# Kernel tuning notes

Hardware: AMD Instinct MI355X
Metric: run time of the kernel (lower is better)

## Reference

```python
import jax, jax.numpy as jnp
import numpy as np

B, N, D, H = 4, 4096, 1024, 16
HD = D // H  # head dim = 64


def setup_inputs() -> dict:
    key = jax.random.key(0)
    k1, k2, k3 = jax.random.split(key, 3)
    x = jax.random.normal(k1, (B, N, D), dtype=jnp.float32)
    Wqkv = jax.random.normal(k2, (3 * D, D), dtype=jnp.float32) * (1.0 / np.sqrt(D))
    Wo = jax.random.normal(k3, (D, D), dtype=jnp.float32) * (1.0 / np.sqrt(D))
    bo = jnp.zeros((D,), dtype=jnp.float32)
    return {"x": x, "Wqkv": Wqkv, "Wo": Wo, "bo": bo}


def reference(x, Wqkv, Wo, bo):
    # qkv projection (no bias): [B,N,3D] -> [B,N,3,H,HD]
    qkv = jnp.einsum('bnd,ed->bne', x, Wqkv).reshape(B, N, 3, H, HD)
    q, k, v = qkv[:, :, 0], qkv[:, :, 1], qkv[:, :, 2]  # each [B,N,H,HD]
    # NOTE: faithful to source — heads are NOT moved to a batch axis, so
    # scores are [B,N,H,H]: attention mixes across heads per token.
    scores = jnp.einsum('bnhd,bngd->bnhg', q, k) / jnp.sqrt(jnp.float32(D))
    w = jax.nn.softmax(scores, axis=-1)            # [B,N,H,H]
    attn = jnp.einsum('bnhg,bngd->bnhd', w, v)     # [B,N,H,HD]
    attn = attn.reshape(B, N, D)
    return jnp.einsum('bnd,ed->bne', attn, Wo) + bo
```

## Files before the change

kernel.cpp:

```cpp
#include <hip/hip_runtime.h>
#include <hip/hip_bf16.h>

using bf16 = __hip_bfloat16;
typedef __attribute__((ext_vector_type(8))) short bf16x8;
typedef __attribute__((ext_vector_type(4))) float f32x4;

#define GLL(gp, lp) __builtin_amdgcn_global_load_lds( \
    (const __attribute__((address_space(1))) void*)(gp), \
    (__attribute__((address_space(3))) void*)(lp), 16, 0, 0)

#define BAR()    asm volatile("s_barrier" ::: "memory")
#define WAITV4() asm volatile("s_waitcnt vmcnt(4)" ::: "memory")
#define WAITV0() asm volatile("s_waitcnt vmcnt(0)" ::: "memory")
#define WAITL0() do { asm volatile("s_waitcnt lgkmcnt(0)" ::: "memory"); \
                      __builtin_amdgcn_sched_barrier(0); } while (0)

__device__ inline short bfbits(float f) {
  union { bf16 h; short s; } u;
  u.h = __float2bfloat16(f);
  return u.s;
}

__device__ inline bf16x8 ldcvt(const float* __restrict__ g) {
  const float4 f0 = *(const float4*)(g);
  const float4 f1 = *(const float4*)(g + 4);
  union { short s[8]; bf16x8 v; } u;
  u.s[0] = bfbits(f0.x); u.s[1] = bfbits(f0.y); u.s[2] = bfbits(f0.z); u.s[3] = bfbits(f0.w);
  u.s[4] = bfbits(f1.x); u.s[5] = bfbits(f1.y); u.s[6] = bfbits(f1.z); u.s[7] = bfbits(f1.w);
  return u.v;
}

__device__ inline void store_c(float* C, size_t idx, float v) { C[idx] = v; }
__device__ inline void store_c(bf16*  C, size_t idx, float v) { C[idx] = __float2bfloat16(v); }

__global__ __launch_bounds__(256)
void f32_to_bf16(const float* __restrict__ src, bf16* __restrict__ dst, int n8) {
  const int i = blockIdx.x * 256 + threadIdx.x;
  if (i < n8) *(bf16x8*)(dst + (size_t)i * 8) = ldcvt(src + (size_t)i * 8);
}

template <typename TB, typename TC>
__global__ __launch_bounds__(256)
void gemm_nt(const bf16* __restrict__ A, const TB* __restrict__ B,
             const float* __restrict__ bias, TC* __restrict__ C,
             int K, int lda, int ldb, int ldc) {
  constexpr bool B_F32 = sizeof(TB) == 4;
  __shared__ __align__(16) bf16 As[128 * 32];
  __shared__ __align__(16) bf16 Bs[128 * 32];
  const int tid  = threadIdx.x;
  const int lane = tid & 63;
  const int wave = tid >> 6;
  const int wm = wave >> 1, wn = wave & 1;
  const int m0 = blockIdx.y * 128;
  const int n0 = blockIdx.x * 128;

  const int srow = wave * 16 + (lane >> 2);
  const int scol = (lane & 3) * 8;
  const bf16* gA0 = A + (size_t)(m0 + srow) * lda + scol;
  const bf16* gA1 = A + (size_t)(m0 + 64 + srow) * lda + scol;
  const TB*   gB0 = B + (size_t)(n0 + srow) * ldb + scol;
  const TB*   gB1 = B + (size_t)(n0 + 64 + srow) * ldb + scol;
  bf16* lA0 = &As[(wave * 16) * 32];
  bf16* lA1 = lA0 + 64 * 32;
  bf16* lB0u = &Bs[(wave * 16) * 32];
  bf16* lB1u = lB0u + 64 * 32;
  bf16* lB0p = &Bs[srow * 32 + scol];
  bf16* lB1p = lB0p + 64 * 32;

  const int fr = lane & 15;
  const int kq = (lane >> 4) * 8;
  f32x4 acc[4][4] = {};

  for (int k0 = 0; k0 < K; k0 += 32) {
    bf16x8 b0, b1;
    if constexpr (B_F32) {
      b0 = ldcvt((const float*)gB0 + k0);
      b1 = ldcvt((const float*)gB1 + k0);
    }
    __syncthreads();
    GLL(gA0 + k0, lA0);
    GLL(gA1 + k0, lA1);
    if constexpr (B_F32) {
      *(bf16x8*)lB0p = b0;
      *(bf16x8*)lB1p = b1;
    } else {
      GLL((const bf16*)gB0 + k0, lB0u);
      GLL((const bf16*)gB1 + k0, lB1u);
    }
    __syncthreads();
    bf16x8 af[4], bfv[4];
#pragma unroll
    for (int t = 0; t < 4; ++t) {
      af[t]  = *(const bf16x8*)&As[(wm * 64 + t * 16 + fr) * 32 + kq];
      bfv[t] = *(const bf16x8*)&Bs[(wn * 64 + t * 16 + fr) * 32 + kq];
    }
#pragma unroll
    for (int i = 0; i < 4; ++i)
#pragma unroll
      for (int j = 0; j < 4; ++j)
        acc[i][j] = __builtin_amdgcn_mfma_f32_16x16x32_bf16(af[i], bfv[j], acc[i][j], 0, 0, 0);
  }

  const int rq  = (lane >> 4) * 4;
  const int col = lane & 15;
#pragma unroll
  for (int j = 0; j < 4; ++j) {
    const int cn = n0 + wn * 64 + j * 16 + col;
    const float bv = bias ? bias[cn] : 0.0f;
#pragma unroll
    for (int i = 0; i < 4; ++i) {
      const int cm = m0 + wm * 64 + i * 16 + rq;
#pragma unroll
      for (int r = 0; r < 4; ++r)
        store_c(C, (size_t)(cm + r) * ldc + cn, acc[i][j][r] + bv);
    }
  }
}

template <typename TC>
__global__ __launch_bounds__(512)
void gemm256(const bf16* __restrict__ A, const bf16* __restrict__ B,
             const float* __restrict__ bias, TC* __restrict__ C,
             int K, int lda, int ldb, int ldc, int nbx) {
  __shared__ __align__(16) bf16 As[2][256][64];
  __shared__ __align__(16) bf16 Bs[2][256][64];
  const int tid  = threadIdx.x;
  const int lane = tid & 63;
  const int wave = tid >> 6;
  const int wm = wave >> 2;
  const int wn = wave & 3;

  int wg = blockIdx.x;
  const int nwg = gridDim.x;
  if ((nwg & 7) == 0) wg = (wg & 7) * (nwg >> 3) + (wg >> 3);
  const int m0 = (wg / nbx) * 256;
  const int n0 = (wg % nbx) * 256;

  const int srow = wave * 8 + (lane >> 3);
  const int scol = ((lane & 7) ^ (lane >> 3)) * 8;
  const bf16* gA = A + (size_t)(m0 + srow) * lda + scol;
  const bf16* gB = B + (size_t)(n0 + srow) * ldb + scol;

  const int fr = lane & 15, quad = lane >> 4, swz = fr & 7;

#define STAGE_A(buf, h, kt) do { \
    GLL(gA + (size_t)((h) * 128     ) * lda + (kt) * 64, &As[buf][(h) * 128      + wave * 8][0]); \
    GLL(gA + (size_t)((h) * 128 + 64) * lda + (kt) * 64, &As[buf][(h) * 128 + 64 + wave * 8][0]); \
  } while (0)
#define STAGE_B(buf, h, kt) do { \
    GLL(gB + (size_t)((h) * 128     ) * ldb + (kt) * 64, &Bs[buf][(h) * 128      + wave * 8][0]); \
    GLL(gB + (size_t)((h) * 128 + 64) * ldb + (kt) * 64, &Bs[buf][(h) * 128 + 64 + wave * 8][0]); \
  } while (0)
#define LDA_G(buf, mh) do { _Pragma("unroll") \
    for (int t = 0; t < 4; ++t) { _Pragma("unroll") \
      for (int ks = 0; ks < 2; ++ks) \
        av[t * 2 + ks] = *(const bf16x8*)&As[buf][wm * 128 + (mh) * 64 + t * 16 + fr] \
                                            [(((ks << 2) | quad) ^ swz) << 3]; } } while (0)
#define LDB_G(buf, nh, dst) do { _Pragma("unroll") \
    for (int t = 0; t < 2; ++t) { _Pragma("unroll") \
      for (int ks = 0; ks < 2; ++ks) \
        dst[t * 2 + ks] = *(const bf16x8*)&Bs[buf][wn * 64 + (nh) * 32 + t * 16 + fr] \
                                             [(((ks << 2) | quad) ^ swz) << 3]; } } while (0)
#define MFMA_Q(mh, nh, bb) do { \
    __builtin_amdgcn_s_setprio(1); \
    _Pragma("unroll") \
    for (int t = 0; t < 4; ++t) { _Pragma("unroll") \
      for (int u = 0; u < 2; ++u) { _Pragma("unroll") \
        for (int ks = 0; ks < 2; ++ks) \
          acc[(mh) * 4 + t][(nh) * 2 + u] = __builtin_amdgcn_mfma_f32_16x16x32_bf16( \
              av[t * 2 + ks], bb[u * 2 + ks], acc[(mh) * 4 + t][(nh) * 2 + u], 0, 0, 0); } } \
    __builtin_amdgcn_s_setprio(0); } while (0)

  bf16x8 av[8], b0[4], b1[4];
  f32x4 acc[8][4] = {};

  STAGE_A(0, 0, 0); STAGE_A(0, 1, 0);
  STAGE_B(0, 0, 0); STAGE_B(0, 1, 0);
  STAGE_B(1, 0, 1); STAGE_B(1, 1, 1);
  WAITV4(); BAR();

  const int KT = K >> 6;
  const int NI = KT >> 1;
  for (int i = 0; i < NI; ++i) {
    const int kt1 = 2 * i + 1;
    const int ka  = (2 * i + 2 < KT) ? 2 * i + 2 : 0;
    const int kb  = (2 * i + 3 < KT) ? 2 * i + 3 : 0;

    LDA_G(0, 0); LDB_G(0, 0, b0); STAGE_A(1, 0, kt1);
    BAR(); WAITL0(); MFMA_Q(0, 0, b0); BAR();
    LDB_G(0, 1, b1); STAGE_A(1, 1, kt1);
    BAR(); WAITL0(); MFMA_Q(0, 1, b1); BAR();
    LDA_G(0, 1); STAGE_B(0, 0, ka);
    BAR(); WAITL0(); MFMA_Q(1, 1, b1); BAR();
    STAGE_B(0, 1, ka); WAITV4();
    BAR(); WAITL0(); MFMA_Q(1, 0, b0); BAR();
    LDA_G(1, 0); LDB_G(1, 0, b0); STAGE_A(0, 0, ka);
    BAR(); WAITL0(); MFMA_Q(0, 0, b0); BAR();
    LDB_G(1, 1, b1); STAGE_A(0, 1, ka);
    BAR(); WAITL0(); MFMA_Q(0, 1, b1); BAR();
    LDA_G(1, 1); STAGE_B(1, 0, kb);
    BAR(); WAITL0(); MFMA_Q(1, 1, b1); BAR();
    STAGE_B(1, 1, kb); WAITV4();
    BAR(); WAITL0(); MFMA_Q(1, 0, b0); BAR();
  }
  WAITV0();

  const int rq = quad * 4;
#pragma unroll
  for (int nj = 0; nj < 4; ++nj) {
    const int cn = n0 + wn * 64 + nj * 16 + fr;
    const float bv = bias ? bias[cn] : 0.0f;
#pragma unroll
    for (int mi = 0; mi < 8; ++mi) {
      const int cm = m0 + wm * 128 + mi * 16 + rq;
#pragma unroll
      for (int r = 0; r < 4; ++r)
        store_c(C, (size_t)(cm + r) * ldc + cn, acc[mi][nj][r] + bv);
    }
  }
#undef STAGE_A
#undef STAGE_B
#undef LDA_G
#undef LDB_G
#undef MFMA_Q
}

__global__ __launch_bounds__(256)
void attn_heads(bf16* __restrict__ qkv) {
  __shared__ __align__(16) bf16  s_qkv[4][3072];
  __shared__ __align__(16) float s_w[4][256];
  const int lane = threadIdx.x & 63;
  const int wave = threadIdx.x >> 6;
  const size_t tok = (size_t)blockIdx.x * 4 + wave;
  bf16* grow = qkv + tok * 3072;

#pragma unroll
  for (int i = 0; i < 6; ++i) {
    const int off = (i * 64 + lane) * 8;
    *(uint4*)(&s_qkv[wave][off]) = *(const uint4*)(&grow[off]);
  }
  __syncthreads();

  const bf16* sq = s_qkv[wave];
  const int fr   = lane & 15;
  const int quad = lane >> 4;

  f32x4 sc = {0.f, 0.f, 0.f, 0.f};
#pragma unroll
  for (int c = 0; c < 2; ++c) {
    bf16x8 a = *(const bf16x8*)&sq[fr * 64 + c * 32 + quad * 8];
    bf16x8 b = *(const bf16x8*)&sq[1024 + fr * 64 + c * 32 + quad * 8];
    sc = __builtin_amdgcn_mfma_f32_16x16x32_bf16(a, b, sc, 0, 0, 0);
  }

#pragma unroll
  for (int r = 0; r < 4; ++r) {
    float s = sc[r] * 0.03125f;
    float mx = s;
#pragma unroll
    for (int msk = 1; msk < 16; msk <<= 1) mx = fmaxf(mx, __shfl_xor(mx, msk, 64));
    float e = __expf(s - mx);
    float sum = e;
#pragma unroll
    for (int msk = 1; msk < 16; msk <<= 1) sum += __shfl_xor(sum, msk, 64);
    s_w[wave][(quad * 4 + r) * 16 + fr] = e / sum;
  }
  __syncthreads();

  float vv[16];
#pragma unroll
  for (int g = 0; g < 16; ++g) vv[g] = __bfloat162float(sq[2048 + g * 64 + lane]);
  const float* wrow = s_w[wave];
#pragma unroll
  for (int h = 0; h < 16; ++h) {
    float o = 0.f;
#pragma unroll
    for (int g4 = 0; g4 < 4; ++g4) {
      f32x4 w4 = *(const f32x4*)&wrow[h * 16 + g4 * 4];
      o += w4.x * vv[g4 * 4 + 0] + w4.y * vv[g4 * 4 + 1] +
           w4.z * vv[g4 * 4 + 2] + w4.w * vv[g4 * 4 + 3];
    }
    grow[h * 64 + lane] = __float2bfloat16(o);
  }
}

extern "C" void kernel_launch(void* const* d_in, const int* in_sizes, int n_in,
                              void* d_out, int out_size, void* d_ws, size_t ws_size,
                              hipStream_t stream) {
  const float* x    = (const float*)d_in[0];
  const float* Wqkv = (const float*)d_in[1];
  const float* Wo   = (const float*)d_in[2];
  const float* bo   = (const float*)d_in[3];
  float* out = (float*)d_out;
  bf16* qkv  = (bf16*)d_ws;

  bf16* xb    = (bf16*)d_out;
  bf16* wqkvb = xb + 16777216;

  const size_t qkv_bytes = (size_t)16384 * 3072 * 2;
  const bool have_ws = ws_size >= qkv_bytes + (size_t)2 * 1024 * 1024;
  bf16* wob = (bf16*)((char*)d_ws + qkv_bytes);

  f32_to_bf16<<<16777216 / 8 / 256, 256, 0, stream>>>(x, xb, 16777216 / 8);
  f32_to_bf16<<<3145728 / 8 / 256, 256, 0, stream>>>(Wqkv, wqkvb, 3145728 / 8);
  if (have_ws)
    f32_to_bf16<<<1048576 / 8 / 256, 256, 0, stream>>>(Wo, wob, 1048576 / 8);

  gemm256<bf16><<<(3072 / 256) * (16384 / 256), 512, 0, stream>>>(
      xb, wqkvb, nullptr, qkv, 1024, 1024, 1024, 3072, 3072 / 256);

  attn_heads<<<dim3(16384 / 4), 256, 0, stream>>>(qkv);

  if (have_ws)
    gemm256<float><<<(1024 / 256) * (16384 / 256), 512, 0, stream>>>(
        qkv, wob, bo, out, 1024, 3072, 1024, 1024, 1024 / 256);
  else
    gemm_nt<float, float><<<dim3(1024 / 128, 16384 / 128), 256, 0, stream>>>(
        qkv, Wo, bo, out, 1024, 3072, 1024, 1024);
}
```

Before: 342.4 us.

## Stage GEMM epilogue through LDS, split QKV into planar buffers, deepen A prefetch

The GEMM epilogue now writes accumulators into swizzled shared memory and then emits coalesced 16-byte global stores, replacing scattered per-element stores. The QKV projection output is split into three separate Q/K/V planes with row stride 1024, and the second GEMM reads attention output with lda 1024 instead of 3072. The converted Wo reuses the V buffer after attention finishes, which removes the fallback path. The GEMM main loop issues one more A stage earlier and adjusts the vmcnt/lgkmcnt waits to hide more load latency, with the A and B buffers merged into a single shared array that the epilogue reuses.

New measurement: 288.7 us. 1.19x faster.

```diff
diff --git a/kernel.cpp b/kernel.cpp
--- a/kernel.cpp
+++ b/kernel.cpp
@@ -11,9 +11,11 @@
 
 #define BAR()    asm volatile("s_barrier" ::: "memory")
 #define WAITV4() asm volatile("s_waitcnt vmcnt(4)" ::: "memory")
+#define WAITV6() asm volatile("s_waitcnt vmcnt(6)" ::: "memory")
 #define WAITV0() asm volatile("s_waitcnt vmcnt(0)" ::: "memory")
 #define WAITL0() do { asm volatile("s_waitcnt lgkmcnt(0)" ::: "memory"); \
                       __builtin_amdgcn_sched_barrier(0); } while (0)
+#define LHINT8() asm volatile("s_waitcnt lgkmcnt(8)" ::: "memory")
 
 __device__ inline short bfbits(float f) {
   union { bf16 h; short s; } u;
@@ -30,100 +32,18 @@
   return u.v;
 }
 
-__device__ inline void store_c(float* C, size_t idx, float v) { C[idx] = v; }
-__device__ inline void store_c(bf16*  C, size_t idx, float v) { C[idx] = __float2bfloat16(v); }
-
 __global__ __launch_bounds__(256)
 void f32_to_bf16(const float* __restrict__ src, bf16* __restrict__ dst, int n8) {
   const int i = blockIdx.x * 256 + threadIdx.x;
   if (i < n8) *(bf16x8*)(dst + (size_t)i * 8) = ldcvt(src + (size_t)i * 8);
 }
 
-template <typename TB, typename TC>
-__global__ __launch_bounds__(256)
-void gemm_nt(const bf16* __restrict__ A, const TB* __restrict__ B,
-             const float* __restrict__ bias, TC* __restrict__ C,
-             int K, int lda, int ldb, int ldc) {
-  constexpr bool B_F32 = sizeof(TB) == 4;
-  __shared__ __align__(16) bf16 As[128 * 32];
-  __shared__ __align__(16) bf16 Bs[128 * 32];
-  const int tid  = threadIdx.x;
-  const int lane = tid & 63;
-  const int wave = tid >> 6;
-  const int wm = wave >> 1, wn = wave & 1;
-  const int m0 = blockIdx.y * 128;
-  const int n0 = blockIdx.x * 128;
-
-  const int srow = wave * 16 + (lane >> 2);
-  const int scol = (lane & 3) * 8;
-  const bf16* gA0 = A + (size_t)(m0 + srow) * lda + scol;
-  const bf16* gA1 = A + (size_t)(m0 + 64 + srow) * lda + scol;
-  const TB*   gB0 = B + (size_t)(n0 + srow) * ldb + scol;
-  const TB*   gB1 = B + (size_t)(n0 + 64 + srow) * ldb + scol;
-  bf16* lA0 = &As[(wave * 16) * 32];
-  bf16* lA1 = lA0 + 64 * 32;
-  bf16* lB0u = &Bs[(wave * 16) * 32];
-  bf16* lB1u = lB0u + 64 * 32;
-  bf16* lB0p = &Bs[srow * 32 + scol];
-  bf16* lB1p = lB0p + 64 * 32;
-
-  const int fr = lane & 15;
-  const int kq = (lane >> 4) * 8;
-  f32x4 acc[4][4] = {};
-
-  for (int k0 = 0; k0 < K; k0 += 32) {
-    bf16x8 b0, b1;
-    if constexpr (B_F32) {
-      b0 = ldcvt((const float*)gB0 + k0);
-      b1 = ldcvt((const float*)gB1 + k0);
-    }
-    __syncthreads();
-    GLL(gA0 + k0, lA0);
-    GLL(gA1 + k0, lA1);
-    if constexpr (B_F32) {
-      *(bf16x8*)lB0p = b0;
-      *(bf16x8*)lB1p = b1;
-    } else {
-      GLL((const bf16*)gB0 + k0, lB0u);
-      GLL((const bf16*)gB1 + k0, lB1u);
-    }
-    __syncthreads();
-    bf16x8 af[4], bfv[4];
-#pragma unroll
-    for (int t = 0; t < 4; ++t) {
-      af[t]  = *(const bf16x8*)&As[(wm * 64 + t * 16 + fr) * 32 + kq];
-      bfv[t] = *(const bf16x8*)&Bs[(wn * 64 + t * 16 + fr) * 32 + kq];
-    }
-#pragma unroll
-    for (int i = 0; i < 4; ++i)
-#pragma unroll
-      for (int j = 0; j < 4; ++j)
-        acc[i][j] = __builtin_amdgcn_mfma_f32_16x16x32_bf16(af[i], bfv[j], acc[i][j], 0, 0, 0);
-  }
-
-  const int rq  = (lane >> 4) * 4;
-  const int col = lane & 15;
-#pragma unroll
-  for (int j = 0; j < 4; ++j) {
-    const int cn = n0 + wn * 64 + j * 16 + col;
-    const float bv = bias ? bias[cn] : 0.0f;
-#pragma unroll
-    for (int i = 0; i < 4; ++i) {
-      const int cm = m0 + wm * 64 + i * 16 + rq;
-#pragma unroll
-      for (int r = 0; r < 4; ++r)
-        store_c(C, (size_t)(cm + r) * ldc + cn, acc[i][j][r] + bv);
-    }
-  }
-}
-
-template <typename TC>
+template <typename TC, bool SPLIT3>
 __global__ __launch_bounds__(512)
 void gemm256(const bf16* __restrict__ A, const bf16* __restrict__ B,
              const float* __restrict__ bias, TC* __restrict__ C,
              int K, int lda, int ldb, int ldc, int nbx) {
-  __shared__ __align__(16) bf16 As[2][256][64];
-  __shared__ __align__(16) bf16 Bs[2][256][64];
+  __shared__ __align__(16) bf16 smem[4][256][64];
   const int tid  = threadIdx.x;
   const int lane = tid & 63;
   const int wave = tid >> 6;
@@ -144,23 +64,23 @@
   const int fr = lane & 15, quad = lane >> 4, swz = fr & 7;
 
 #define STAGE_A(buf, h, kt) do { \
-    GLL(gA + (size_t)((h) * 128     ) * lda + (kt) * 64, &As[buf][(h) * 128      + wave * 8][0]); \
-    GLL(gA + (size_t)((h) * 128 + 64) * lda + (kt) * 64, &As[buf][(h) * 128 + 64 + wave * 8][0]); \
+    GLL(gA + (size_t)((h) * 128     ) * lda + (kt) * 64, &smem[buf][(h) * 128      + wave * 8][0]); \
+    GLL(gA + (size_t)((h) * 128 + 64) * lda + (kt) * 64, &smem[buf][(h) * 128 + 64 + wave * 8][0]); \
   } while (0)
 #define STAGE_B(buf, h, kt) do { \
-    GLL(gB + (size_t)((h) * 128     ) * ldb + (kt) * 64, &Bs[buf][(h) * 128      + wave * 8][0]); \
-    GLL(gB + (size_t)((h) * 128 + 64) * ldb + (kt) * 64, &Bs[buf][(h) * 128 + 64 + wave * 8][0]); \
+    GLL(gB + (size_t)((h) * 128     ) * ldb + (kt) * 64, &smem[2 + (buf)][(h) * 128      + wave * 8][0]); \
+    GLL(gB + (size_t)((h) * 128 + 64) * ldb + (kt) * 64, &smem[2 + (buf)][(h) * 128 + 64 + wave * 8][0]); \
   } while (0)
 #define LDA_G(buf, mh) do { _Pragma("unroll") \
     for (int t = 0; t < 4; ++t) { _Pragma("unroll") \
       for (int ks = 0; ks < 2; ++ks) \
-        av[t * 2 + ks] = *(const bf16x8*)&As[buf][wm * 128 + (mh) * 64 + t * 16 + fr] \
-                                            [(((ks << 2) | quad) ^ swz) << 3]; } } while (0)
+        av[t * 2 + ks] = *(const bf16x8*)&smem[buf][wm * 128 + (mh) * 64 + t * 16 + fr] \
+                                             [(((ks << 2) | quad) ^ swz) << 3]; } } while (0)
 #define LDB_G(buf, nh, dst) do { _Pragma("unroll") \
     for (int t = 0; t < 2; ++t) { _Pragma("unroll") \
       for (int ks = 0; ks < 2; ++ks) \
-        dst[t * 2 + ks] = *(const bf16x8*)&Bs[buf][wn * 64 + (nh) * 32 + t * 16 + fr] \
-                                             [(((ks << 2) | quad) ^ swz) << 3]; } } while (0)
+        dst[t * 2 + ks] = *(const bf16x8*)&smem[2 + (buf)][wn * 64 + (nh) * 32 + t * 16 + fr] \
+                                              [(((ks << 2) | quad) ^ swz) << 3]; } } while (0)
 #define MFMA_Q(mh, nh, bb) do { \
     __builtin_amdgcn_s_setprio(1); \
     _Pragma("unroll") \
@@ -177,7 +97,8 @@
   STAGE_A(0, 0, 0); STAGE_A(0, 1, 0);
   STAGE_B(0, 0, 0); STAGE_B(0, 1, 0);
   STAGE_B(1, 0, 1); STAGE_B(1, 1, 1);
-  WAITV4(); BAR();
+  STAGE_A(1, 0, 1);
+  WAITV6(); BAR();
 
   const int KT = K >> 6;
   const int NI = KT >> 1;
@@ -186,36 +107,93 @@
     const int ka  = (2 * i + 2 < KT) ? 2 * i + 2 : 0;
     const int kb  = (2 * i + 3 < KT) ? 2 * i + 3 : 0;
 
-    LDA_G(0, 0); LDB_G(0, 0, b0); STAGE_A(1, 0, kt1);
+    LDA_G(0, 0); LDB_G(0, 0, b0); STAGE_A(1, 1, kt1);
+    LHINT8();
     BAR(); WAITL0(); MFMA_Q(0, 0, b0); BAR();
-    LDB_G(0, 1, b1); STAGE_A(1, 1, kt1);
+    LDB_G(0, 1, b1);
     BAR(); WAITL0(); MFMA_Q(0, 1, b1); BAR();
     LDA_G(0, 1); STAGE_B(0, 0, ka);
     BAR(); WAITL0(); MFMA_Q(1, 1, b1); BAR();
     STAGE_B(0, 1, ka); WAITV4();
     BAR(); WAITL0(); MFMA_Q(1, 0, b0); BAR();
     LDA_G(1, 0); LDB_G(1, 0, b0); STAGE_A(0, 0, ka);
+    LHINT8();
     BAR(); WAITL0(); MFMA_Q(0, 0, b0); BAR();
     LDB_G(1, 1, b1); STAGE_A(0, 1, ka);
     BAR(); WAITL0(); MFMA_Q(0, 1, b1); BAR();
     LDA_G(1, 1); STAGE_B(1, 0, kb);
     BAR(); WAITL0(); MFMA_Q(1, 1, b1); BAR();
-    STAGE_B(1, 1, kb); WAITV4();
+    STAGE_B(1, 1, kb); STAGE_A(1, 0, kb); WAITV6();
     BAR(); WAITL0(); MFMA_Q(1, 0, b0); BAR();
   }
-  WAITV0();
+  WAITV0(); BAR();
 
   const int rq = quad * 4;
-#pragma unroll
-  for (int nj = 0; nj < 4; ++nj) {
-    const int cn = n0 + wn * 64 + nj * 16 + fr;
-    const float bv = bias ? bias[cn] : 0.0f;
-#pragma unroll
-    for (int mi = 0; mi < 8; ++mi) {
-      const int cm = m0 + wm * 128 + mi * 16 + rq;
-#pragma unroll
-      for (int r = 0; r < 4; ++r)
-        store_c(C, (size_t)(cm + r) * ldc + cn, acc[mi][nj][r] + bv);
+  char* myc = (char*)(&smem[0][0][0]) + wave * 16384;
+  float bvv[4];
+#pragma unroll
+  for (int nj = 0; nj < 4; ++nj)
+    bvv[nj] = bias ? bias[n0 + wn * 64 + nj * 16 + fr] : 0.0f;
+
+  const int cn0 = n0 + wn * 64;
+
+  if constexpr (sizeof(TC) == 2) {
+#pragma unroll
+    for (int mi = 0; mi < 8; ++mi)
+#pragma unroll
+      for (int nj = 0; nj < 4; ++nj)
+#pragma unroll
+        for (int r = 0; r < 4; ++r) {
+          const int row   = mi * 16 + rq + r;
+          const int chunk = ((nj << 1) | (fr >> 3)) ^ (row & 7);
+          *(short*)(myc + row * 128 + chunk * 16 + (fr & 7) * 2) =
+              bfbits(acc[mi][nj][r] + bvv[nj]);
+        }
+    asm volatile("s_waitcnt lgkmcnt(0)" ::: "memory");
+    __builtin_amdgcn_sched_barrier(0);
+    const int rr = lane >> 3, rc = (lane & 7) ^ (lane >> 3);
+    size_t cbase;
+    if constexpr (SPLIT3)
+      cbase = ((size_t)(cn0 >> 10) << 24) + (size_t)(m0 + wm * 128) * 1024 + (cn0 & 1023);
+    else
+      cbase = (size_t)(m0 + wm * 128) * ldc + cn0;
+    const int cstride = SPLIT3 ? 1024 : ldc;
+#pragma unroll
+    for (int j = 0; j < 16; ++j) {
+      const int row = j * 8 + rr;
+      const uint4 d = *(const uint4*)(myc + row * 128 + rc * 16);
+      *(uint4*)((bf16*)C + cbase + (size_t)row * cstride + (lane & 7) * 8) = d;
+    }
+  } else {
+#pragma unroll
+    for (int p = 0; p < 2; ++p) {
+#pragma unroll
+      for (int mi = 0; mi < 4; ++mi)
+#pragma unroll
+        for (int nj = 0; nj < 4; ++nj)
+#pragma unroll
+          for (int r = 0; r < 4; ++r) {
+            const int row   = mi * 16 + rq + r;
+            const int col   = nj * 16 + fr;
+            const int chunk = (col >> 2) ^ (row & 7);
+            *(float*)(myc + row * 256 + chunk * 16 + (col & 3) * 4) =
+                acc[p * 4 + mi][nj][r] + bvv[nj];
+          }
+      asm volatile("s_waitcnt lgkmcnt(0)" ::: "memory");
+      __builtin_amdgcn_sched_barrier(0);
+      const int rr = lane >> 4, rc0 = lane & 15;
+#pragma unroll
+      for (int j = 0; j < 16; ++j) {
+        const int row   = j * 4 + rr;
+        const int chunk = rc0 ^ (row & 7);
+        const uint4 d = *(const uint4*)(myc + row * 256 + chunk * 16);
+        *(uint4*)((float*)C + (size_t)(m0 + wm * 128 + p * 64 + row) * ldc
+                  + cn0 + rc0 * 4) = d;
+      }
+      if (p == 0) {
+        asm volatile("s_waitcnt lgkmcnt(0)" ::: "memory");
+        __builtin_amdgcn_sched_barrier(0);
+      }
     }
   }
 #undef STAGE_A
@@ -226,18 +204,23 @@
 }
 
 __global__ __launch_bounds__(256)
-void attn_heads(bf16* __restrict__ qkv) {
+void attn_heads(bf16* __restrict__ qp, const bf16* __restrict__ kp,
+                const bf16* __restrict__ vp) {
   __shared__ __align__(16) bf16  s_qkv[4][3072];
   __shared__ __align__(16) float s_w[4][256];
   const int lane = threadIdx.x & 63;
   const int wave = threadIdx.x >> 6;
   const size_t tok = (size_t)blockIdx.x * 4 + wave;
-  bf16* grow = qkv + tok * 3072;
-
-#pragma unroll
-  for (int i = 0; i < 6; ++i) {
+  bf16*       qrow = qp + tok * 1024;
+  const bf16* krow = kp + tok * 1024;
+  const bf16* vrow = vp + tok * 1024;
+
+#pragma unroll
+  for (int i = 0; i < 2; ++i) {
     const int off = (i * 64 + lane) * 8;
-    *(uint4*)(&s_qkv[wave][off]) = *(const uint4*)(&grow[off]);
+    *(uint4*)(&s_qkv[wave][off])        = *(const uint4*)(qrow + off);
+    *(uint4*)(&s_qkv[wave][1024 + off]) = *(const uint4*)(krow + off);
+    *(uint4*)(&s_qkv[wave][2048 + off]) = *(const uint4*)(vrow + off);
   }
   __syncthreads();
 
@@ -280,7 +263,7 @@
       o += w4.x * vv[g4 * 4 + 0] + w4.y * vv[g4 * 4 + 1] +
            w4.z * vv[g4 * 4 + 2] + w4.w * vv[g4 * 4 + 3];
     }
-    grow[h * 64 + lane] = __float2bfloat16(o);
+    qrow[h * 64 + lane] = __float2bfloat16(o);
   }
 }
 
@@ -291,30 +274,24 @@
   const float* Wqkv = (const float*)d_in[1];
   const float* Wo   = (const float*)d_in[2];
   const float* bo   = (const float*)d_in[3];
-  float* out = (float*)d_out;
-  bf16* qkv  = (bf16*)d_ws;
+
+  bf16* qp = (bf16*)d_ws;
+  bf16* kp = qp + ((size_t)1 << 24);
+  bf16* vp = qp + ((size_t)2 << 24);
 
   bf16* xb    = (bf16*)d_out;
   bf16* wqkvb = xb + 16777216;
 
-  const size_t qkv_bytes = (size_t)16384 * 3072 * 2;
-  const bool have_ws = ws_size >= qkv_bytes + (size_t)2 * 1024 * 1024;
-  bf16* wob = (bf16*)((char*)d_ws + qkv_bytes);
-
-  f32_to_bf16<<<16777216 / 8 / 256, 256, 0, stream>>>(x, xb, 16777216 / 8);
-  f32_to_bf16<<<3145728 / 8 / 256, 256, 0, stream>>>(Wqkv, wqkvb, 3145728 / 8);
-  if (have_ws)
-    f32_to_bf16<<<1048576 / 8 / 256, 256, 0, stream>>>(Wo, wob, 1048576 / 8);
-
-  gemm256<bf16><<<(3072 / 256) * (16384 / 256), 512, 0, stream>>>(
-      xb, wqkvb, nullptr, qkv, 1024, 1024, 1024, 3072, 3072 / 256);
-
-  attn_heads<<<dim3(16384 / 4), 256, 0, stream>>>(qkv);
-
-  if (have_ws)
-    gemm256<float><<<(1024 / 256) * (16384 / 256), 512, 0, stream>>>(
-        qkv, wob, bo, out, 1024, 3072, 1024, 1024, 1024 / 256);
-  else
-    gemm_nt<float, float><<<dim3(1024 / 128, 16384 / 128), 256, 0, stream>>>(
-        qkv, Wo, bo, out, 1024, 3072, 1024, 1024);
-}
+  f32_to_bf16<<<8192, 256, 0, stream>>>(x, xb, 2097152);
+  f32_to_bf16<<<1536, 256, 0, stream>>>(Wqkv, wqkvb, 393216);
+
+  gemm256<bf16, true><<<768, 512, 0, stream>>>(
+      xb, wqkvb, nullptr, qp, 1024, 1024, 1024, 1024, 12);
+
+  attn_heads<<<4096, 256, 0, stream>>>(qp, kp, vp);
+
+  f32_to_bf16<<<512, 256, 0, stream>>>(Wo, vp, 131072);
+
+  gemm256<float, false><<<256, 512, 0, stream>>>(
+      qp, vp, bo, (float*)d_out, 1024, 1024, 1024, 1024, 4);
+}
```
